# Optimization experiments

Hardware: AMD Instinct MI355X
Metric: run time of the kernel (lower is better)

Reference implementation:

```python
import jax, jax.numpy as jnp
import numpy as np

B, C, T = 128, 272, 1024
D1, K = 270, 32


def setup_inputs() -> dict:
    key = jax.random.key(0)
    k1, k2, k3, k4 = jax.random.split(key, 4)
    X = jax.random.normal(k1, (B, C, T), dtype=jnp.float32)
    loc = jax.random.uniform(k2, (C, 2), dtype=jnp.float32)  # 2D sensor coords in [0,1]
    z_re = jax.random.normal(k3, (D1, K, K), dtype=jnp.float32)
    z_im = jax.random.normal(k4, (D1, K, K), dtype=jnp.float32)
    return {"X": X, "loc": loc, "z_re": z_re, "z_im": z_im}


def reference(X, loc, z_re, z_im):
    # X: [B, C, T]; loc: [C, 2]; z_re/z_im: [D1, K, K]
    Kdim = z_re.shape[1]
    x, y = loc[:, 0], loc[:, 1]                      # [C]
    k = jnp.arange(Kdim, dtype=X.dtype)
    # phase[k, l, c] = 2*pi*(k*x[c] + l*y[c])
    phase = 2.0 * jnp.pi * (k[:, None, None] * x[None, None, :]
                            + k[None, :, None] * y[None, None, :])  # [K, K, C]
    # a[j, c] = sum_{k,l} z_re[j,k,l]*cos(phase) + z_im[j,k,l]*sin(phase)
    A = (jnp.einsum('dkl,klc->dc', z_re, jnp.cos(phase))
         + jnp.einsum('dkl,klc->dc', z_im, jnp.sin(phase)))  # [D1, C]
    # exp(a_j) / sum_c exp(a_j) == softmax over channels (same math)
    w = jax.nn.softmax(A, axis=1)                    # [D1, C]
    # out[b, j, t] = sum_c w[j,c] * X[b,c,t]
    return jnp.einsum('dc,bct->bdt', w, X)           # [B, D1, T]
```

## Files before the change

kernel.cpp:

```cpp
#include <hip/hip_runtime.h>

#define BB 128
#define CC 272
#define TT 1024
#define DD 270
#define KK 32
#define NKC 9
#define NMT 17
#define MP 272
#define WUNITS ((NKC * NMT * 1024) / 16)

typedef __attribute__((ext_vector_type(8))) short s16x8;
typedef __attribute__((ext_vector_type(4))) float f32x4;

__device__ __forceinline__ unsigned short f2bf(float f) {
  unsigned int u = __builtin_bit_cast(unsigned int, f);
  u += 0x7fffu + ((u >> 16) & 1u);
  return (unsigned short)(u >> 16);
}

__global__ __launch_bounds__(288) void phaseA_kernel(
    const float* __restrict__ loc, const float* __restrict__ z_re,
    const float* __restrict__ z_im, float* __restrict__ A) {
  const int d = blockIdx.x;
  const int p = blockIdx.y;
  const int c = threadIdx.x;
  if (c >= CC) return;
  const float TWO_PI = 6.28318530717958647692f;
  float x = loc[2 * c], y = loc[2 * c + 1];
  float sx, cx, sy, cyv;
  sincosf(TWO_PI * x, &sx, &cx);
  sincosf(TWO_PI * y, &sy, &cyv);
  float cl[KK], sl[KK];
  cl[0] = 1.f; sl[0] = 0.f;
#pragma unroll
  for (int l = 1; l < KK; ++l) {
    cl[l] = cl[l - 1] * cyv - sl[l - 1] * sy;
    sl[l] = sl[l - 1] * cyv + cl[l - 1] * sy;
  }
  const int k0 = p * 8;
  float sk, ck;
  sincosf(TWO_PI * (float)k0 * x, &sk, &ck);
  const float* zr = z_re + (size_t)d * (KK * KK) + k0 * KK;
  const float* zi = z_im + (size_t)d * (KK * KK) + k0 * KK;
  float acc = 0.f;
  for (int k = 0; k < 8; ++k) {
    float s_rc = 0.f, s_rs = 0.f, s_ic = 0.f, s_is = 0.f;
#pragma unroll
    for (int l = 0; l < KK; ++l) {
      float vr = zr[k * KK + l];
      float vi = zi[k * KK + l];
      s_rc += vr * cl[l];
      s_rs += vr * sl[l];
      s_ic += vi * cl[l];
      s_is += vi * sl[l];
    }
    acc += ck * (s_rc + s_is) + sk * (s_ic - s_rs);
    float nck = ck * cx - sk * sx;
    sk = sk * cx + ck * sx;
    ck = nck;
  }
  atomicAdd(&A[d * CC + c], acc);
}

__global__ __launch_bounds__(64) void softmax_kernel(
    const float* __restrict__ A, unsigned short* __restrict__ wb) {
  const int d = blockIdx.x;
  const int lane = threadIdx.x;
  const bool live = (d < DD);
  float v[5];
  float inv = 0.f;
  if (live) {
    float m = -3.0e38f;
#pragma unroll
    for (int j = 0; j < 5; ++j) {
      int cidx = lane + 64 * j;
      v[j] = (cidx < CC) ? A[(size_t)d * CC + cidx] : -3.0e38f;
      m = fmaxf(m, v[j]);
    }
#pragma unroll
    for (int off = 32; off >= 1; off >>= 1) m = fmaxf(m, __shfl_xor(m, off, 64));
    float s = 0.f;
#pragma unroll
    for (int j = 0; j < 5; ++j) {
      int cidx = lane + 64 * j;
      v[j] = (cidx < CC) ? expf(v[j] - m) : 0.f;
      s += v[j];
    }
#pragma unroll
    for (int off = 32; off >= 1; off >>= 1) s += __shfl_xor(s, off, 64);
    inv = 1.f / s;
  }
  const int mt = d >> 4, mrow = d & 15;
#pragma unroll
  for (int j = 0; j < 5; ++j) {
    int kk = lane + 64 * j;
    if (kk < NKC * KK) {
      unsigned short val = 0;
      if (live && kk < CC) val = f2bf(v[j] * inv);
      int kc = kk >> 5, hi = (kk >> 3) & 3, jj = kk & 7;
      wb[((size_t)(kc * NMT + mt) << 9) + (((hi << 4) | mrow) << 3) + jj] = val;
    }
  }
}

__global__ __launch_bounds__(512, 2) void gemm_kernel(
    const float* __restrict__ X, const unsigned short* __restrict__ wb,
    float* __restrict__ out) {
  __shared__ unsigned short wlds[NKC * NMT * 512];
  const int bid = blockIdx.x;
  const int L = (bid & 7) * 64 + (bid >> 3);
  const int b = L >> 2;
  const int t0 = (L & 3) << 8;
  const int tid = threadIdx.x;
  const int lane = tid & 63;
  const int wv = tid >> 6;
  const int q = lane >> 4;
  const int r16 = lane & 15;
  const int csub = q << 3;

  {
    const char* src = (const char*)wb;
    char* dst = (char*)wlds;
#pragma unroll
    for (int r = 0; r < 20; ++r) {
      int idx = tid + r * 512;
      if (idx < WUNITS) {
        __builtin_amdgcn_global_load_lds(
            (const __attribute__((address_space(1))) unsigned int*)(src + idx * 16),
            (__attribute__((address_space(3))) unsigned int*)(dst + idx * 16),
            16, 0, 0);
      }
    }
  }

  f32x4 acc[NMT][2];
#pragma unroll
  for (int i = 0; i < NMT; ++i)
#pragma unroll
    for (int f = 0; f < 2; ++f) acc[i][f] = (f32x4){0.f, 0.f, 0.f, 0.f};

  const float* Xb = X + (size_t)b * (CC * TT) + t0 + wv * 32 + r16;

#define XLOAD(DST, KC)                                                  \
  {                                                                     \
    _Pragma("unroll") for (int j = 0; j < 8; ++j) {                     \
      int c_ = (KC) * KK + csub + j;                                    \
      float v0_ = 0.f, v1_ = 0.f;                                       \
      if ((KC) < 8 || c_ < CC) {                                        \
        v0_ = Xb[(size_t)c_ * TT];                                      \
        v1_ = Xb[(size_t)c_ * TT + 16];                                 \
      }                                                                 \
      DST[j] = v0_;                                                     \
      DST[8 + j] = v1_;                                                 \
    }                                                                   \
  }

  float x0[16], x1[16], x2[16];
  XLOAD(x0, 0);
  XLOAD(x1, 1);
  XLOAD(x2, 2);

  __syncthreads();

#define BODY(KC, XC)                                                          \
  {                                                                           \
    union { unsigned int u[4]; s16x8 v; } bf[2];                              \
    _Pragma("unroll") for (int f = 0; f < 2; ++f)                             \
        _Pragma("unroll") for (int p = 0; p < 4; ++p)                         \
        bf[f].u[p] = (unsigned int)f2bf(XC[f * 8 + 2 * p]) |                  \
                     ((unsigned int)f2bf(XC[f * 8 + 2 * p + 1]) << 16);       \
    if ((KC) + 3 < NKC) { XLOAD(XC, (KC) + 3); }                              \
    const char* wch_ = (const char*)wlds + (size_t)(KC) * (NMT * 1024) +      \
                       (size_t)lane * 16;                                     \
    _Pragma("unroll") for (int mt = 0; mt < NMT; ++mt) {                      \
      s16x8 af_ = *(const s16x8*)(wch_ + mt * 1024);                          \
      acc[mt][0] = __builtin_amdgcn_mfma_f32_16x16x32_bf16(af_, bf[0].v,      \
                                                           acc[mt][0], 0, 0, 0); \
      acc[mt][1] = __builtin_amdgcn_mfma_f32_16x16x32_bf16(af_, bf[1].v,      \
                                                           acc[mt][1], 0, 0, 0); \
    }                                                                         \
  }

  BODY(0, x0) BODY(1, x1) BODY(2, x2)
  BODY(3, x0) BODY(4, x1) BODY(5, x2)
  BODY(6, x0) BODY(7, x1) BODY(8, x2)

#undef BODY
#undef XLOAD

  float* op = out + (size_t)b * (DD * TT) + t0 + wv * 32 + r16;
#pragma unroll
  for (int mt = 0; mt < NMT; ++mt) {
#pragma unroll
    for (int f = 0; f < 2; ++f)
#pragma unroll
      for (int r = 0; r < 4; ++r) {
        const int drow = mt * 16 + q * 4 + r;
        if (drow < DD) op[(size_t)drow * TT + (f << 4)] = acc[mt][f][r];
      }
  }
}

extern "C" void kernel_launch(void* const* d_in, const int* in_sizes, int n_in,
                              void* d_out, int out_size, void* d_ws, size_t ws_size,
                              hipStream_t stream) {
  const float* X = (const float*)d_in[0];
  const float* loc = (const float*)d_in[1];
  const float* z_re = (const float*)d_in[2];
  const float* z_im = (const float*)d_in[3];
  float* out = (float*)d_out;

  float* A = (float*)d_ws;
  unsigned short* wbf = (unsigned short*)((char*)d_ws + 294912);

  hipMemsetAsync(A, 0, DD * CC * sizeof(float), stream);
  phaseA_kernel<<<dim3(DD, 4), 288, 0, stream>>>(loc, z_re, z_im, A);
  softmax_kernel<<<MP, 64, 0, stream>>>(A, wbf);
  gemm_kernel<<<BB * (TT / 256), 512, 0, stream>>>(X, wbf, out);
}
```

Baseline: 309.1 us.

## Fuse phase and softmax kernels; vectorize X loads and output stores to float2

Measured after the change: 283.2 us. 8.4% less time.

```diff
diff --git a/kernel.cpp b/kernel.cpp
--- a/kernel.cpp
+++ b/kernel.cpp
@@ -7,11 +7,11 @@
 #define KK 32
 #define NKC 9
 #define NMT 17
-#define MP 272
 #define WUNITS ((NKC * NMT * 1024) / 16)
 
 typedef __attribute__((ext_vector_type(8))) short s16x8;
 typedef __attribute__((ext_vector_type(4))) float f32x4;
+typedef __attribute__((ext_vector_type(2))) float f32x2;
 
 __device__ __forceinline__ unsigned short f2bf(float f) {
   unsigned int u = __builtin_bit_cast(unsigned int, f);
@@ -19,88 +19,75 @@
   return (unsigned short)(u >> 16);
 }
 
-__global__ __launch_bounds__(288) void phaseA_kernel(
+__global__ __launch_bounds__(320) void phaseA_softmax_kernel(
     const float* __restrict__ loc, const float* __restrict__ z_re,
-    const float* __restrict__ z_im, float* __restrict__ A) {
+    const float* __restrict__ z_im, unsigned short* __restrict__ wb) {
   const int d = blockIdx.x;
-  const int p = blockIdx.y;
-  const int c = threadIdx.x;
-  if (c >= CC) return;
+  const int tid = threadIdx.x;
+  const int c = tid;
+  const bool live = (d < DD) && (c < CC);
   const float TWO_PI = 6.28318530717958647692f;
-  float x = loc[2 * c], y = loc[2 * c + 1];
-  float sx, cx, sy, cyv;
-  sincosf(TWO_PI * x, &sx, &cx);
-  sincosf(TWO_PI * y, &sy, &cyv);
-  float cl[KK], sl[KK];
-  cl[0] = 1.f; sl[0] = 0.f;
-#pragma unroll
-  for (int l = 1; l < KK; ++l) {
-    cl[l] = cl[l - 1] * cyv - sl[l - 1] * sy;
-    sl[l] = sl[l - 1] * cyv + cl[l - 1] * sy;
-  }
-  const int k0 = p * 8;
-  float sk, ck;
-  sincosf(TWO_PI * (float)k0 * x, &sk, &ck);
-  const float* zr = z_re + (size_t)d * (KK * KK) + k0 * KK;
-  const float* zi = z_im + (size_t)d * (KK * KK) + k0 * KK;
+
   float acc = 0.f;
-  for (int k = 0; k < 8; ++k) {
-    float s_rc = 0.f, s_rs = 0.f, s_ic = 0.f, s_is = 0.f;
-#pragma unroll
-    for (int l = 0; l < KK; ++l) {
-      float vr = zr[k * KK + l];
-      float vi = zi[k * KK + l];
-      s_rc += vr * cl[l];
-      s_rs += vr * sl[l];
-      s_ic += vi * cl[l];
-      s_is += vi * sl[l];
-    }
-    acc += ck * (s_rc + s_is) + sk * (s_ic - s_rs);
-    float nck = ck * cx - sk * sx;
-    sk = sk * cx + ck * sx;
-    ck = nck;
-  }
-  atomicAdd(&A[d * CC + c], acc);
-}
-
-__global__ __launch_bounds__(64) void softmax_kernel(
-    const float* __restrict__ A, unsigned short* __restrict__ wb) {
-  const int d = blockIdx.x;
-  const int lane = threadIdx.x;
-  const bool live = (d < DD);
-  float v[5];
-  float inv = 0.f;
   if (live) {
-    float m = -3.0e38f;
-#pragma unroll
-    for (int j = 0; j < 5; ++j) {
-      int cidx = lane + 64 * j;
-      v[j] = (cidx < CC) ? A[(size_t)d * CC + cidx] : -3.0e38f;
-      m = fmaxf(m, v[j]);
-    }
-#pragma unroll
-    for (int off = 32; off >= 1; off >>= 1) m = fmaxf(m, __shfl_xor(m, off, 64));
-    float s = 0.f;
-#pragma unroll
-    for (int j = 0; j < 5; ++j) {
-      int cidx = lane + 64 * j;
-      v[j] = (cidx < CC) ? expf(v[j] - m) : 0.f;
-      s += v[j];
-    }
-#pragma unroll
-    for (int off = 32; off >= 1; off >>= 1) s += __shfl_xor(s, off, 64);
-    inv = 1.f / s;
-  }
-  const int mt = d >> 4, mrow = d & 15;
-#pragma unroll
-  for (int j = 0; j < 5; ++j) {
-    int kk = lane + 64 * j;
-    if (kk < NKC * KK) {
-      unsigned short val = 0;
-      if (live && kk < CC) val = f2bf(v[j] * inv);
-      int kc = kk >> 5, hi = (kk >> 3) & 3, jj = kk & 7;
-      wb[((size_t)(kc * NMT + mt) << 9) + (((hi << 4) | mrow) << 3) + jj] = val;
-    }
+    float x = loc[2 * c], y = loc[2 * c + 1];
+    float sx, cx, sy, cyv;
+    sincosf(TWO_PI * x, &sx, &cx);
+    sincosf(TWO_PI * y, &sy, &cyv);
+    float cl[KK], sl[KK];
+    cl[0] = 1.f; sl[0] = 0.f;
+#pragma unroll
+    for (int l = 1; l < KK; ++l) {
+      cl[l] = cl[l - 1] * cyv - sl[l - 1] * sy;
+      sl[l] = sl[l - 1] * cyv + cl[l - 1] * sy;
+    }
+    for (int p = 0; p < 4; ++p) {
+      const int k0 = p * 8;
+      float sk, ck;
+      sincosf(TWO_PI * (float)k0 * x, &sk, &ck);
+      const float* zr = z_re + (size_t)d * (KK * KK) + k0 * KK;
+      const float* zi = z_im + (size_t)d * (KK * KK) + k0 * KK;
+      for (int k = 0; k < 8; ++k) {
+        float s_rc = 0.f, s_rs = 0.f, s_ic = 0.f, s_is = 0.f;
+#pragma unroll
+        for (int l = 0; l < KK; ++l) {
+          float vr = zr[k * KK + l];
+          float vi = zi[k * KK + l];
+          s_rc += vr * cl[l];
+          s_rs += vr * sl[l];
+          s_ic += vi * cl[l];
+          s_is += vi * sl[l];
+        }
+        acc += ck * (s_rc + s_is) + sk * (s_ic - s_rs);
+        float nck = ck * cx - sk * sx;
+        sk = sk * cx + ck * sx;
+        ck = nck;
+      }
+    }
+  }
+
+  __shared__ float redm[5], reds[5];
+  float m = live ? acc : -3.0e38f;
+#pragma unroll
+  for (int off = 32; off >= 1; off >>= 1) m = fmaxf(m, __shfl_xor(m, off, 64));
+  if ((tid & 63) == 0) redm[tid >> 6] = m;
+  __syncthreads();
+  const float mAll = fmaxf(fmaxf(fmaxf(redm[0], redm[1]),
+                                 fmaxf(redm[2], redm[3])), redm[4]);
+  float e = live ? expf(acc - mAll) : 0.f;
+  float s = e;
+#pragma unroll
+  for (int off = 32; off >= 1; off >>= 1) s += __shfl_xor(s, off, 64);
+  if ((tid & 63) == 0) reds[tid >> 6] = s;
+  __syncthreads();
+  const float sAll = reds[0] + reds[1] + reds[2] + reds[3] + reds[4];
+  const float inv = 1.f / sAll;
+
+  if (c < NKC * KK) {
+    unsigned short val = live ? f2bf(e * inv) : (unsigned short)0;
+    const int mt = d >> 4, mrow = d & 15;
+    const int kc = c >> 5, hi = (c >> 3) & 3, jj = c & 7;
+    wb[((size_t)(kc * NMT + mt) << 9) + (((hi << 4) | mrow) << 3) + jj] = val;
   }
 }
 
@@ -140,19 +127,17 @@
 #pragma unroll
     for (int f = 0; f < 2; ++f) acc[i][f] = (f32x4){0.f, 0.f, 0.f, 0.f};
 
-  const float* Xb = X + (size_t)b * (CC * TT) + t0 + wv * 32 + r16;
+  const float* Xb = X + (size_t)b * (CC * TT) + t0 + wv * 32 + 2 * r16;
 
 #define XLOAD(DST, KC)                                                  \
   {                                                                     \
     _Pragma("unroll") for (int j = 0; j < 8; ++j) {                     \
       int c_ = (KC) * KK + csub + j;                                    \
-      float v0_ = 0.f, v1_ = 0.f;                                       \
-      if ((KC) < 8 || c_ < CC) {                                        \
-        v0_ = Xb[(size_t)c_ * TT];                                      \
-        v1_ = Xb[(size_t)c_ * TT + 16];                                 \
-      }                                                                 \
-      DST[j] = v0_;                                                     \
-      DST[8 + j] = v1_;                                                 \
+      f32x2 v_ = (f32x2){0.f, 0.f};                                     \
+      if ((KC) < 8 || c_ < CC)                                          \
+        v_ = *(const f32x2*)(Xb + (size_t)c_ * TT);                     \
+      DST[j] = v_[0];                                                   \
+      DST[8 + j] = v_[1];                                               \
     }                                                                   \
   }
 
@@ -189,16 +174,17 @@
 #undef BODY
 #undef XLOAD
 
-  float* op = out + (size_t)b * (DD * TT) + t0 + wv * 32 + r16;
+  float* op = out + (size_t)b * (DD * TT) + t0 + wv * 32 + 2 * r16;
 #pragma unroll
   for (int mt = 0; mt < NMT; ++mt) {
 #pragma unroll
-    for (int f = 0; f < 2; ++f)
-#pragma unroll
-      for (int r = 0; r < 4; ++r) {
-        const int drow = mt * 16 + q * 4 + r;
-        if (drow < DD) op[(size_t)drow * TT + (f << 4)] = acc[mt][f][r];
+    for (int r = 0; r < 4; ++r) {
+      const int drow = mt * 16 + q * 4 + r;
+      if (drow < DD) {
+        f32x2 st = (f32x2){acc[mt][0][r], acc[mt][1][r]};
+        *(f32x2*)(op + (size_t)drow * TT) = st;
       }
+    }
   }
 }
 
@@ -211,11 +197,8 @@
   const float* z_im = (const float*)d_in[3];
   float* out = (float*)d_out;
 
-  float* A = (float*)d_ws;
-  unsigned short* wbf = (unsigned short*)((char*)d_ws + 294912);
-
-  hipMemsetAsync(A, 0, DD * CC * sizeof(float), stream);
-  phaseA_kernel<<<dim3(DD, 4), 288, 0, stream>>>(loc, z_re, z_im, A);
-  softmax_kernel<<<MP, 64, 0, stream>>>(A, wbf);
+  unsigned short* wbf = (unsigned short*)d_ws;
+
+  phaseA_softmax_kernel<<<NMT * 16, 320, 0, stream>>>(loc, z_re, z_im, wbf);
   gemm_kernel<<<BB * (TT / 256), 512, 0, stream>>>(X, wbf, out);
 }
```
